# Kernel tuning notes

Measured on AMD Instinct MI355X. Metric: run time of the kernel, lower is better.

Reference implementation:

```python
import jax, jax.numpy as jnp
import numpy as np

K = 10          # number of clusters (static; matches randint fill_max)
ALPHA = 0.02    # intra-cluster margin
DELTA = 0.5     # inter-cluster margin
LAMBDA_INTRA = 1.0
LAMBDA_INTER = 1.0
MIN_WEIGHT = 50.0


def setup_inputs() -> dict:
    key = jax.random.key(0)
    k1, k2 = jax.random.split(key)
    x = jax.random.normal(k1, (8, 64, 240, 320), dtype=jnp.float32)
    # module assumes NORMALIZED unit vectors along channel dim
    x = x / jnp.maximum(jnp.linalg.norm(x, axis=1, keepdims=True), 1e-12)
    cluster_masks = jax.random.randint(k2, (8, 1, 240, 320), 0, K, dtype=jnp.int32)
    return {"x": x, "cluster_masks": cluster_masks}


def reference(x, cluster_masks):
    B, C, H, W = x.shape
    cm = cluster_masks[:, 0]  # (B, H, W) int
    # one-hot cluster assignment; out-of-range ids (e.g. -1 = unlabeled) -> all zeros
    onehot = jax.nn.one_hot(cm, K, dtype=x.dtype)  # (B, H, W, K)

    # ---- spherical cluster means (fused segment-reduce over H*W) ----
    sums = jnp.einsum('bchw,bhwk->bck', x, onehot)          # (B, C, K)
    counts = jnp.sum(onehot, axis=(1, 2))                    # (B, K)
    means = sums / (counts[:, None, :] + 1e-10)
    # F.normalize(p=2, dim=1): x / max(||x||, eps)
    means = means / jnp.maximum(jnp.linalg.norm(means, axis=1, keepdims=True), 1e-12)

    # ---- broadcast means back to pixels ----
    tiled = jnp.einsum('bck,bhwk->bchw', means, onehot)      # (B, C, H, W)

    labeled = (cm >= 0).astype(x.dtype)                      # (B, H, W)
    # cosine metric
    intra_d = labeled * (0.5 * (1.0 - jnp.sum(x * tiled, axis=1)))  # (B, H, W)

    # ---- per-cluster hard-example weighting ----
    indicator = (intra_d > ALPHA).astype(x.dtype)            # (B, H, W)
    N_k = jnp.einsum('bhw,bhwk->bk', indicator, onehot)      # (B, K)
    weights = jnp.einsum('bk,bhwk->bhw', N_k, onehot)        # (B, H, W)
    weights = jnp.maximum(weights, MIN_WEIGHT) * K
    intra_loss = jnp.sum(intra_d ** 2 / weights) / B
    intra_loss = LAMBDA_INTRA * jnp.where(jnp.sum(indicator) > 0, intra_loss, 0.0)

    # ---- inter-cluster hinge loss (K > 1 statically) ----
    inter_d = 0.5 * (1.0 - jnp.einsum('bck,bcl->bkl', means, means))  # (B, K, K)
    hinge = jnp.maximum(DELTA - inter_d, 0.0) * (1.0 - jnp.eye(K, dtype=x.dtype))
    inter_loss = LAMBDA_INTER * jnp.sum(hinge ** 2) / (K * (K - 1) / 2 * B)

    loss = intra_loss + inter_loss
    return (loss, intra_loss, inter_loss)
```

## Files before the change

kernel.cpp:

```cpp
#include <hip/hip_runtime.h>
#include <hip/hip_bf16.h>

#define B_ 8
#define C_ 64
#define H_ 240
#define W_ 320
#define HW_ (H_ * W_)
#define HW4_ (HW_ / 4)
#define K_ 10
#define ALPHA_ 0.02f
#define DELTA_ 0.5f
#define MIN_WEIGHT_ 50.0f

#define K1_SPLIT 8


__global__ __launch_bounds__(256) void k1_sums(
    const float* __restrict__ x, const int* __restrict__ cm,
    float* __restrict__ sums, float* __restrict__ counts) {
  const int c = blockIdx.x;
  const int b = blockIdx.y;
  const int z = blockIdx.z;
  const int tid = threadIdx.x;

  const int chunk = HW4_ / K1_SPLIT;
  const int lo = z * chunk;
  const int hi = lo + chunk;

  const float4* __restrict__ xp =
      (const float4*)(x + (size_t)(b * C_ + c) * HW_);
  const int4* __restrict__ cp = (const int4*)(cm + (size_t)b * HW_);

  float acc[K_];
#pragma unroll
  for (int j = 0; j < K_; ++j) acc[j] = 0.f;
  float cnt[K_];
#pragma unroll
  for (int j = 0; j < K_; ++j) cnt[j] = 0.f;
  const bool do_cnt = (c == 0);

  for (int i = lo + tid; i < hi; i += 256) {
    float4 v = xp[i];
    int4 k4 = cp[i];
#pragma unroll
    for (int j = 0; j < K_; ++j) {
      acc[j] += (k4.x == j ? v.x : 0.f);
      acc[j] += (k4.y == j ? v.y : 0.f);
      acc[j] += (k4.z == j ? v.z : 0.f);
      acc[j] += (k4.w == j ? v.w : 0.f);
    }
    if (do_cnt) {
#pragma unroll
      for (int j = 0; j < K_; ++j) {
        cnt[j] += (float)((k4.x == j) + (k4.y == j) + (k4.z == j) + (k4.w == j));
      }
    }
  }

#pragma unroll
  for (int j = 0; j < K_; ++j) {
    float v = acc[j];
#pragma unroll
    for (int off = 32; off > 0; off >>= 1) v += __shfl_down(v, off, 64);
    if ((tid & 63) == 0) atomicAdd(&sums[(b * C_ + c) * K_ + j], v);
  }
  if (do_cnt) {
#pragma unroll
    for (int j = 0; j < K_; ++j) {
      float v = cnt[j];
#pragma unroll
      for (int off = 32; off > 0; off >>= 1) v += __shfl_down(v, off, 64);
      if ((tid & 63) == 0) atomicAdd(&counts[b * K_ + j], v);
    }
  }
}

__global__ __launch_bounds__(256) void k3_intra(
    const float* __restrict__ x, const int* __restrict__ cm,
    const float* __restrict__ sums, const float* __restrict__ counts,
    float* __restrict__ means, float* __restrict__ S2,
    float* __restrict__ Nk, float* __restrict__ indtot) {
  const int b = blockIdx.y;
  const int chunk = blockIdx.x;
  const int tid = threadIdx.x;
  const int lane_p = tid & 63;
  const int grp = tid >> 6;

  __shared__ float mlds[C_ * K_];
  __shared__ float nrm[K_];
  __shared__ float4 pd[256];
  __shared__ float s2b[K_];
  __shared__ float nkb[K_];

  for (int i = tid; i < C_ * K_; i += 256) {
    const int k = i % K_;
    mlds[i] = sums[b * C_ * K_ + i] / (counts[b * K_ + k] + 1e-10f);
  }
  if (tid < K_) { s2b[tid] = 0.f; nkb[tid] = 0.f; }
  __syncthreads();
  if (tid < K_) {
    float n2 = 0.f;
#pragma unroll
    for (int c = 0; c < C_; ++c) {
      const float mm = mlds[c * K_ + tid];
      n2 += mm * mm;
    }
    nrm[tid] = 1.f / fmaxf(sqrtf(n2), 1e-12f);
  }
  __syncthreads();
  for (int i = tid; i < C_ * K_; i += 256) mlds[i] *= nrm[i % K_];
  __syncthreads();
  if (chunk == 0) {
    for (int i = tid; i < C_ * K_; i += 256) means[b * C_ * K_ + i] = mlds[i];
  }

  const int p4 = chunk * 64 + lane_p;
  const int4 k4 = ((const int4*)(cm + (size_t)b * HW_))[p4];
  const float4* __restrict__ xb = (const float4*)(x + (size_t)b * C_ * HW_);

  float d0 = 0.f, d1 = 0.f, d2 = 0.f, d3 = 0.f;
  const int c0 = grp * (C_ / 4);
#pragma unroll
  for (int cc = 0; cc < C_ / 4; ++cc) {
    const int c = c0 + cc;
    float4 v = xb[c * HW4_ + p4];
    const float* mr = &mlds[c * K_];
    d0 += v.x * mr[k4.x];
    d1 += v.y * mr[k4.y];
    d2 += v.z * mr[k4.z];
    d3 += v.w * mr[k4.w];
  }
  pd[tid] = make_float4(d0, d1, d2, d3);
  __syncthreads();

  if (grp == 0) {
    float4 a = pd[lane_p];
    float4 bb = pd[lane_p + 64];
    float4 cc = pd[lane_p + 128];
    float4 dd = pd[lane_p + 192];
    const float i0 = 0.5f * (1.f - (a.x + bb.x + cc.x + dd.x));
    const float i1 = 0.5f * (1.f - (a.y + bb.y + cc.y + dd.y));
    const float i2 = 0.5f * (1.f - (a.z + bb.z + cc.z + dd.z));
    const float i3 = 0.5f * (1.f - (a.w + bb.w + cc.w + dd.w));

    atomicAdd(&s2b[k4.x], i0 * i0);
    atomicAdd(&s2b[k4.y], i1 * i1);
    atomicAdd(&s2b[k4.z], i2 * i2);
    atomicAdd(&s2b[k4.w], i3 * i3);
    atomicAdd(&nkb[k4.x], i0 > ALPHA_ ? 1.f : 0.f);
    atomicAdd(&nkb[k4.y], i1 > ALPHA_ ? 1.f : 0.f);
    atomicAdd(&nkb[k4.z], i2 > ALPHA_ ? 1.f : 0.f);
    atomicAdd(&nkb[k4.w], i3 > ALPHA_ ? 1.f : 0.f);
  }
  __syncthreads();

  if (tid < K_) {
    atomicAdd(&S2[b * K_ + tid], s2b[tid]);
    atomicAdd(&Nk[b * K_ + tid], nkb[tid]);
    atomicAdd(indtot, nkb[tid]);
  }
}

__global__ __launch_bounds__(256) void k4_final(
    const float* __restrict__ means, const float* __restrict__ S2,
    const float* __restrict__ Nk, const float* __restrict__ indtot,
    float* __restrict__ out) {
  const int tid = threadIdx.x;

  float h2 = 0.f;
  for (int t = tid; t < B_ * 45; t += 256) {
    const int b = t / 45;
    int idx = t % 45;
    int k = 0, l = 0;
    for (k = 0; k < K_; ++k) {
      const int row = K_ - 1 - k;
      if (idx < row) { l = k + 1 + idx; break; }
      idx -= row;
    }
    float g = 0.f;
    for (int c = 0; c < C_; ++c)
      g += means[(b * C_ + c) * K_ + k] * means[(b * C_ + c) * K_ + l];
    const float inter_d = 0.5f * (1.f - g);
    const float h = fmaxf(DELTA_ - inter_d, 0.f);
    h2 += 2.f * h * h;
  }

  __shared__ float red[256];
  red[tid] = h2;
  __syncthreads();
  for (int s = 128; s > 0; s >>= 1) {
    if (tid < s) red[tid] += red[tid + s];
    __syncthreads();
  }
  if (tid == 0) {
    const float inter = red[0] / (float)((K_ * (K_ - 1) / 2) * B_);
    float intra = 0.f;
    for (int i = 0; i < B_ * K_; ++i) {
      const float w = fmaxf(Nk[i], MIN_WEIGHT_) * (float)K_;
      intra += S2[i] / w;
    }
    intra /= (float)B_;
    if (!(indtot[0] > 0.f)) intra = 0.f;
    out[0] = intra + inter;
    out[1] = intra;
    out[2] = inter;
  }
}

extern "C" void kernel_launch(void* const* d_in, const int* in_sizes, int n_in,
                              void* d_out, int out_size, void* d_ws, size_t ws_size,
                              hipStream_t stream) {
  const float* x = (const float*)d_in[0];
  const int* cm = (const int*)d_in[1];

  float* ws = (float*)d_ws;
  float* sums = ws;
  float* counts = ws + 5120;
  float* means = ws + 5200;
  float* S2 = ws + 10320;
  float* Nk = ws + 10400;
  float* indtot = ws + 10480;

  hipMemsetAsync(d_ws, 0, 10481 * sizeof(float), stream);

  k1_sums<<<dim3(C_, B_, K1_SPLIT), 256, 0, stream>>>(x, cm, sums, counts);
  k3_intra<<<dim3(HW4_ / 64, B_), 256, 0, stream>>>(x, cm, sums, counts, means,
                                                    S2, Nk, indtot);
  k4_final<<<1, 256, 0, stream>>>(means, S2, Nk, indtot, (float*)d_out);
}
```

Baseline: 295.7 us.

## Process four channels per block in sums kernel and drop global indicator atomic

The sums kernel now gives each block four channels. The cluster one-hot is decoded once per int4 of labels and reused for all four channels, which cuts redundant label loads and compare work and reduces the grid by four. The intra kernel hoists per-lane LDS mean pointers out of the loop. The global indtot atomic is removed; the final kernel instead derives the indicator total from Nk with a parallel reduction, which also shrinks the memset. In exchange there are more accumulator registers (40 acc plus 40 one-hot values) and fewer blocks, which may lower occupancy.

```diff
diff --git a/kernel.cpp b/kernel.cpp
--- a/kernel.cpp
+++ b/kernel.cpp
@@ -1,5 +1,4 @@
 #include <hip/hip_runtime.h>
-#include <hip/hip_bf16.h>
 
 #define B_ 8
 #define C_ 64
@@ -12,57 +11,79 @@
 #define DELTA_ 0.5f
 #define MIN_WEIGHT_ 50.0f
 
-#define K1_SPLIT 8
+#define NCH 4
+#define CB_ (C_ / NCH)
+#define Z1 8
 
 
 __global__ __launch_bounds__(256) void k1_sums(
     const float* __restrict__ x, const int* __restrict__ cm,
     float* __restrict__ sums, float* __restrict__ counts) {
-  const int c = blockIdx.x;
+  const int cb = blockIdx.x;
   const int b = blockIdx.y;
   const int z = blockIdx.z;
   const int tid = threadIdx.x;
-
-  const int chunk = HW4_ / K1_SPLIT;
+  const int c0 = cb * NCH;
+
+  const int chunk = HW4_ / Z1;
   const int lo = z * chunk;
   const int hi = lo + chunk;
 
   const float4* __restrict__ xp =
-      (const float4*)(x + (size_t)(b * C_ + c) * HW_);
+      (const float4*)(x + (size_t)(b * C_ + c0) * HW_);
   const int4* __restrict__ cp = (const int4*)(cm + (size_t)b * HW_);
 
-  float acc[K_];
-#pragma unroll
-  for (int j = 0; j < K_; ++j) acc[j] = 0.f;
+  float acc[NCH][K_];
+#pragma unroll
+  for (int c = 0; c < NCH; ++c)
+#pragma unroll
+    for (int j = 0; j < K_; ++j) acc[c][j] = 0.f;
+
   float cnt[K_];
 #pragma unroll
   for (int j = 0; j < K_; ++j) cnt[j] = 0.f;
-  const bool do_cnt = (c == 0);
+  const bool do_cnt = (cb == 0);
 
   for (int i = lo + tid; i < hi; i += 256) {
-    float4 v = xp[i];
-    int4 k4 = cp[i];
+    const int4 k4 = cp[i];
+
+    float oh0[K_], oh1[K_], oh2[K_], oh3[K_];
 #pragma unroll
     for (int j = 0; j < K_; ++j) {
-      acc[j] += (k4.x == j ? v.x : 0.f);
-      acc[j] += (k4.y == j ? v.y : 0.f);
-      acc[j] += (k4.z == j ? v.z : 0.f);
-      acc[j] += (k4.w == j ? v.w : 0.f);
+      oh0[j] = (k4.x == j) ? 1.f : 0.f;
+      oh1[j] = (k4.y == j) ? 1.f : 0.f;
+      oh2[j] = (k4.z == j) ? 1.f : 0.f;
+      oh3[j] = (k4.w == j) ? 1.f : 0.f;
     }
     if (do_cnt) {
 #pragma unroll
+      for (int j = 0; j < K_; ++j)
+        cnt[j] += (oh0[j] + oh1[j]) + (oh2[j] + oh3[j]);
+    }
+
+#pragma unroll
+    for (int c = 0; c < NCH; ++c) {
+      const float4 v = xp[c * HW4_ + i];
+#pragma unroll
       for (int j = 0; j < K_; ++j) {
-        cnt[j] += (float)((k4.x == j) + (k4.y == j) + (k4.z == j) + (k4.w == j));
+        acc[c][j] += v.x * oh0[j];
+        acc[c][j] += v.y * oh1[j];
+        acc[c][j] += v.z * oh2[j];
+        acc[c][j] += v.w * oh3[j];
       }
     }
   }
 
 #pragma unroll
-  for (int j = 0; j < K_; ++j) {
-    float v = acc[j];
-#pragma unroll
-    for (int off = 32; off > 0; off >>= 1) v += __shfl_down(v, off, 64);
-    if ((tid & 63) == 0) atomicAdd(&sums[(b * C_ + c) * K_ + j], v);
+  for (int c = 0; c < NCH; ++c) {
+#pragma unroll
+    for (int j = 0; j < K_; ++j) {
+      float v = acc[c][j];
+#pragma unroll
+      for (int off = 32; off > 0; off >>= 1) v += __shfl_down(v, off, 64);
+      if ((tid & 63) == 0)
+        atomicAdd(&sums[(b * C_ + c0 + c) * K_ + j], v);
+    }
   }
   if (do_cnt) {
 #pragma unroll
@@ -79,7 +100,7 @@
     const float* __restrict__ x, const int* __restrict__ cm,
     const float* __restrict__ sums, const float* __restrict__ counts,
     float* __restrict__ means, float* __restrict__ S2,
-    float* __restrict__ Nk, float* __restrict__ indtot) {
+    float* __restrict__ Nk) {
   const int b = blockIdx.y;
   const int chunk = blockIdx.x;
   const int tid = threadIdx.x;
@@ -118,17 +139,20 @@
   const int4 k4 = ((const int4*)(cm + (size_t)b * HW_))[p4];
   const float4* __restrict__ xb = (const float4*)(x + (size_t)b * C_ * HW_);
 
+  const int c0 = grp * (C_ / 4);
+  const float* __restrict__ m0 = &mlds[c0 * K_ + k4.x];
+  const float* __restrict__ m1 = &mlds[c0 * K_ + k4.y];
+  const float* __restrict__ m2 = &mlds[c0 * K_ + k4.z];
+  const float* __restrict__ m3 = &mlds[c0 * K_ + k4.w];
+
   float d0 = 0.f, d1 = 0.f, d2 = 0.f, d3 = 0.f;
-  const int c0 = grp * (C_ / 4);
 #pragma unroll
   for (int cc = 0; cc < C_ / 4; ++cc) {
-    const int c = c0 + cc;
-    float4 v = xb[c * HW4_ + p4];
-    const float* mr = &mlds[c * K_];
-    d0 += v.x * mr[k4.x];
-    d1 += v.y * mr[k4.y];
-    d2 += v.z * mr[k4.z];
-    d3 += v.w * mr[k4.w];
+    const float4 v = xb[(c0 + cc) * HW4_ + p4];
+    d0 += v.x * m0[cc * K_];
+    d1 += v.y * m1[cc * K_];
+    d2 += v.z * m2[cc * K_];
+    d3 += v.w * m3[cc * K_];
   }
   pd[tid] = make_float4(d0, d1, d2, d3);
   __syncthreads();
@@ -157,17 +181,15 @@
   if (tid < K_) {
     atomicAdd(&S2[b * K_ + tid], s2b[tid]);
     atomicAdd(&Nk[b * K_ + tid], nkb[tid]);
-    atomicAdd(indtot, nkb[tid]);
   }
 }
 
 __global__ __launch_bounds__(256) void k4_final(
     const float* __restrict__ means, const float* __restrict__ S2,
-    const float* __restrict__ Nk, const float* __restrict__ indtot,
-    float* __restrict__ out) {
+    const float* __restrict__ Nk, float* __restrict__ out) {
   const int tid = threadIdx.x;
 
-  float h2 = 0.f;
+  float acc_h = 0.f;
   for (int t = tid; t < B_ * 45; t += 256) {
     const int b = t / 45;
     int idx = t % 45;
@@ -182,25 +204,35 @@
       g += means[(b * C_ + c) * K_ + k] * means[(b * C_ + c) * K_ + l];
     const float inter_d = 0.5f * (1.f - g);
     const float h = fmaxf(DELTA_ - inter_d, 0.f);
-    h2 += 2.f * h * h;
-  }
-
-  __shared__ float red[256];
-  red[tid] = h2;
+    acc_h += 2.f * h * h;
+  }
+
+  float acc_i = 0.f;
+  float acc_n = 0.f;
+  if (tid < B_ * K_) {
+    const float nk = Nk[tid];
+    acc_n = nk;
+    const float w = fmaxf(nk, MIN_WEIGHT_) * (float)K_;
+    acc_i = S2[tid] / w;
+  }
+
+  __shared__ float rh[256], ri[256], rn[256];
+  rh[tid] = acc_h;
+  ri[tid] = acc_i;
+  rn[tid] = acc_n;
   __syncthreads();
   for (int s = 128; s > 0; s >>= 1) {
-    if (tid < s) red[tid] += red[tid + s];
+    if (tid < s) {
+      rh[tid] += rh[tid + s];
+      ri[tid] += ri[tid + s];
+      rn[tid] += rn[tid + s];
+    }
     __syncthreads();
   }
   if (tid == 0) {
-    const float inter = red[0] / (float)((K_ * (K_ - 1) / 2) * B_);
-    float intra = 0.f;
-    for (int i = 0; i < B_ * K_; ++i) {
-      const float w = fmaxf(Nk[i], MIN_WEIGHT_) * (float)K_;
-      intra += S2[i] / w;
-    }
-    intra /= (float)B_;
-    if (!(indtot[0] > 0.f)) intra = 0.f;
+    const float inter = rh[0] / (float)((K_ * (K_ - 1) / 2) * B_);
+    float intra = ri[0] / (float)B_;
+    if (!(rn[0] > 0.f)) intra = 0.f;
     out[0] = intra + inter;
     out[1] = intra;
     out[2] = inter;
@@ -216,15 +248,14 @@
   float* ws = (float*)d_ws;
   float* sums = ws;
   float* counts = ws + 5120;
-  float* means = ws + 5200;
-  float* S2 = ws + 10320;
-  float* Nk = ws + 10400;
-  float* indtot = ws + 10480;
-
-  hipMemsetAsync(d_ws, 0, 10481 * sizeof(float), stream);
-
-  k1_sums<<<dim3(C_, B_, K1_SPLIT), 256, 0, stream>>>(x, cm, sums, counts);
+  float* S2 = ws + 5200;
+  float* Nk = ws + 5280;
+  float* means = ws + 5360;
+
+  hipMemsetAsync(d_ws, 0, 5360 * sizeof(float), stream);
+
+  k1_sums<<<dim3(CB_, B_, Z1), 256, 0, stream>>>(x, cm, sums, counts);
   k3_intra<<<dim3(HW4_ / 64, B_), 256, 0, stream>>>(x, cm, sums, counts, means,
-                                                    S2, Nk, indtot);
-  k4_final<<<1, 256, 0, stream>>>(means, S2, Nk, indtot, (float*)d_out);
-}
+                                                    S2, Nk);
+  k4_final<<<1, 256, 0, stream>>>(means, S2, Nk, (float*)d_out);
+}
```

Result: faster. 285.9 us (-3.3%).
